# Kernel tuning notes

Measured on AMD Instinct MI355X. Metric: run time of the kernel, lower is better.

## Reference

```python
import jax, jax.numpy as jnp
import numpy as np

N_NODES = 100000
N_EDGES = 1600000
F_IN = 65
HIDDEN = 128
N_CLASSES = 32
NEG_SLOPE = 0.2


def _gat_conv(x0, src, dst, W, a_src, a_dst, b):
    """Single-head GAT-style conv: gather over edges, segment softmax, scatter-add."""
    h = x0 @ W                                  # [N, C]
    s = h @ a_src                                # [N]
    d = h @ a_dst                                # [N]
    e = jax.nn.leaky_relu(s[src] + d[dst], NEG_SLOPE)   # [E]
    m = jax.ops.segment_max(e, dst, num_segments=N_NODES)
    m = jnp.where(jnp.isfinite(m), m, 0.0)
    ex = jnp.exp(e - m[dst])                     # [E]
    denom = jax.ops.segment_sum(ex, dst, num_segments=N_NODES)
    alpha = ex / (denom[dst] + 1e-16)            # [E]
    out = jax.ops.segment_sum(h[src] * alpha[:, None], dst, num_segments=N_NODES)
    return out + b                               # [N, C]


def setup_inputs() -> dict:
    key = jax.random.key(0)
    ks = jax.random.split(key, 12)
    sc_in = 1.0 / np.sqrt(F_IN)
    sc_h = 1.0 / np.sqrt(HIDDEN)
    return {
        "x": jax.random.normal(ks[0], (N_NODES, F_IN), dtype=jnp.float32),
        "edge_index": jax.random.randint(ks[1], (2, N_EDGES), 0, N_NODES, dtype=jnp.int64),
        "W_mlp": jax.random.normal(ks[2], (F_IN, HIDDEN), dtype=jnp.float32) * sc_in,
        "b_mlp": jnp.zeros((HIDDEN,), dtype=jnp.float32),
        "W1": jax.random.normal(ks[3], (HIDDEN, N_CLASSES), dtype=jnp.float32) * sc_h,
        "a1_src": jax.random.normal(ks[4], (N_CLASSES,), dtype=jnp.float32) * 0.1,
        "a1_dst": jax.random.normal(ks[5], (N_CLASSES,), dtype=jnp.float32) * 0.1,
        "b1": jnp.zeros((N_CLASSES,), dtype=jnp.float32),
        "W2": jax.random.normal(ks[6], (HIDDEN, N_CLASSES), dtype=jnp.float32) * sc_h,
        "a2_src": jax.random.normal(ks[7], (N_CLASSES,), dtype=jnp.float32) * 0.1,
        "a2_dst": jax.random.normal(ks[8], (N_CLASSES,), dtype=jnp.float32) * 0.1,
        "b2": jnp.zeros((N_CLASSES,), dtype=jnp.float32),
    }


def reference(x, edge_index, W_mlp, b_mlp, W1, a1_src, a1_dst, b1, W2, a2_src, a2_dst, b2):
    src, dst = edge_index[0], edge_index[1]
    x0 = jax.nn.relu(x @ W_mlp + b_mlp)                      # [N, H]
    x1 = jax.nn.relu(_gat_conv(x0, src, dst, W1, a1_src, a1_dst, b1))  # [N, C]
    # dropout is identity in eval mode
    x2 = _gat_conv(x0, src, dst, W2, a2_src, a2_dst, b2)     # [N, C]
    x3 = jnp.max(x0, axis=-1, keepdims=True)                 # [N, 1]
    lngal_out = jnp.concatenate((x1, x2, x3), axis=-1) + x   # [N, 2C+1] == [N, F]
    return jax.nn.log_softmax(lngal_out, axis=1)
```

## Files before the change

### kernel.cpp

```cpp
#include <hip/hip_runtime.h>
#include <hip/hip_bf16.h>

#define NN 100000
#define NE 1600000
#define FIN 65
#define HID 128
#define NC 32
#define OUTC 65
#define NBUCK 391
#define CHUNKS 400
#define CH 4000
#define ESTRIDE 5120
#define NODE_BLOCKS 1563

typedef __attribute__((ext_vector_type(8))) short s8v;
typedef __attribute__((ext_vector_type(4))) float f4v;
#define MFMA16(a, b, c) __builtin_amdgcn_mfma_f32_16x16x32_bf16(a, b, c, 0, 0, 0)

__device__ __forceinline__ float lrelu(float v){ return v > 0.f ? v : 0.2f * v; }
__device__ __forceinline__ short f2bs(float f){
  unsigned u = __float_as_uint(f);
  u += 0x7fffu + ((u >> 16) & 1u);
  return (short)(u >> 16);
}
__device__ __forceinline__ float bfu_lo(unsigned u){ return __uint_as_float(u << 16); }
__device__ __forceinline__ float bfu_hi(unsigned u){ return __uint_as_float(u & 0xffff0000u); }

__global__ __launch_bounds__(256) void k_prep(
    const float* __restrict__ Wmlp, const float* __restrict__ W1,
    const float* __restrict__ W2, short* __restrict__ wbg,
    int* __restrict__ bcursor)
{
  const int i = blockIdx.x * 256 + threadIdx.x;
  if (blockIdx.x == 0)
    for (int t = threadIdx.x; t < NBUCK; t += 256) bcursor[t] = 0;
  {
    const int j = i & 7, l = (i >> 3) & 63, nt = (i >> 9) & 7, t = i >> 12;
    const int k = t * 32 + ((l >> 4) << 3) + j;
    const int col = (nt << 4) + (l & 15);
    wbg[i] = f2bs(Wmlp[k * HID + col]);
  }
  {
    const int j = i & 7, l = (i >> 3) & 63, nt = (i >> 9) & 3, t = i >> 11;
    const int k = t * 32 + ((l >> 4) << 3) + j;
    const int col = (nt << 4) + (l & 15);
    wbg[8192 + i] = f2bs(col < NC ? W1[k * NC + col] : W2[k * NC + col - NC]);
  }
}

__global__ __launch_bounds__(256) void k_main(
    const float* __restrict__ x, const short* __restrict__ wbg,
    const float* __restrict__ Wmlp, const float* __restrict__ bmlp,
    const float* __restrict__ a1s, const float* __restrict__ a1d,
    const float* __restrict__ a2s, const float* __restrict__ a2d,
    const int* __restrict__ ei,
    unsigned short* __restrict__ hb16,
    float* __restrict__ sd2, float* __restrict__ dd2,
    float* __restrict__ out,
    int* __restrict__ bcursor, int* __restrict__ ebuf)
{
  __shared__ alignas(16) char smem[28416];
  const int tid = threadIdx.x;

  if (blockIdx.x >= NODE_BLOCKS) {
    const int cb = blockIdx.x - NODE_BLOCKS;
    int* lh = (int*)smem;
    int* lbase = lh + NBUCK;
    for (int i = tid; i < NBUCK; i += 256) lh[i] = 0;
    __syncthreads();
    const int4* s4 = (const int4*)ei + cb * (CH / 4);
    const int4* d4 = (const int4*)(ei + NE) + cb * (CH / 4);
    for (int i = tid; i < CH / 4; i += 256) {
      int4 v = d4[i];
      atomicAdd(&lh[v.x >> 8], 1);
      atomicAdd(&lh[v.y >> 8], 1);
      atomicAdd(&lh[v.z >> 8], 1);
      atomicAdd(&lh[v.w >> 8], 1);
    }
    __syncthreads();
    for (int i = tid; i < NBUCK; i += 256) {
      int c = lh[i];
      lbase[i] = c ? (i * ESTRIDE + atomicAdd(&bcursor[i], c)) : 0;
      lh[i] = 0;
    }
    __syncthreads();
    for (int i = tid; i < CH / 4; i += 256) {
      int4 sv = s4[i];
      int4 dv = d4[i];
      int b, r;
      b = dv.x >> 8; r = atomicAdd(&lh[b], 1); ebuf[lbase[b] + r] = (sv.x << 8) | (dv.x & 255);
      b = dv.y >> 8; r = atomicAdd(&lh[b], 1); ebuf[lbase[b] + r] = (sv.y << 8) | (dv.y & 255);
      b = dv.z >> 8; r = atomicAdd(&lh[b], 1); ebuf[lbase[b] + r] = (sv.z << 8) | (dv.z & 255);
      b = dv.w >> 8; r = atomicAdd(&lh[b], 1); ebuf[lbase[b] + r] = (sv.w << 8) | (dv.w & 255);
    }
    return;
  }

  short* xbf = (short*)smem;
  short* x0b = (short*)(smem + 9216);
  float* xc64 = (float*)(smem + 26624);
  float* w64 = (float*)(smem + 26880);
  float* bmv = (float*)(smem + 27392);
  float* avv = (float*)(smem + 27904);

  const int base = blockIdx.x * 64;

  if (tid < 128) { w64[tid] = Wmlp[64 * HID + tid]; bmv[tid] = bmlp[tid]; }
  else if (tid < 160) {
    const int q = tid - 128;
    avv[q] = a1s[q]; avv[32 + q] = a1d[q]; avv[64 + q] = a2s[q]; avv[96 + q] = a2d[q];
  }
  for (int i = tid; i < 64 * 65; i += 256) {
    const int r = i / 65, c = i - r * 65;
    const int node = base + r;
    const float v = (node < NN) ? x[(size_t)node * FIN + c] : 0.f;
    if (c == 64) xc64[r] = v; else xbf[r * 72 + c] = f2bs(v);
  }
  __syncthreads();

  const int w = tid >> 6, lane = tid & 63;
  const int g = lane >> 4, q = lane & 15;
  const int rowA = w * 16 + q;
  const int rowD0 = w * 16 + g * 4;
  const s8v* wv8 = (const s8v*)wbg;

  const s8v a0 = *(const s8v*)&xbf[rowA * 72 + g * 8];
  const s8v a1 = *(const s8v*)&xbf[rowA * 72 + 32 + g * 8];

  f4v acc[8];
  #pragma unroll
  for (int nt = 0; nt < 8; ++nt) acc[nt] = (f4v){0.f, 0.f, 0.f, 0.f};
  #pragma unroll
  for (int nt = 0; nt < 8; ++nt) {
    const s8v b0 = wv8[nt * 64 + lane];
    const s8v b1 = wv8[(8 + nt) * 64 + lane];
    acc[nt] = MFMA16(a0, b0, acc[nt]);
    acc[nt] = MFMA16(a1, b1, acc[nt]);
  }

  float xc[4];
  #pragma unroll
  for (int r = 0; r < 4; ++r) xc[r] = xc64[rowD0 + r];
  float rmax[4] = {0.f, 0.f, 0.f, 0.f};
  #pragma unroll
  for (int nt = 0; nt < 8; ++nt) {
    const int col = nt * 16 + q;
    const float wvv = w64[col], bv = bmv[col];
    #pragma unroll
    for (int r = 0; r < 4; ++r) {
      const float v = fmaxf(fmaf(xc[r], wvv, acc[nt][r]) + bv, 0.f);
      rmax[r] = fmaxf(rmax[r], v);
      x0b[(rowD0 + r) * 136 + col] = f2bs(v);
    }
  }
  #pragma unroll
  for (int off = 1; off < 16; off <<= 1)
    #pragma unroll
    for (int r = 0; r < 4; ++r) rmax[r] = fmaxf(rmax[r], __shfl_xor(rmax[r], off));
  if (q == 0) {
    #pragma unroll
    for (int r = 0; r < 4; ++r) {
      const int node = base + rowD0 + r;
      if (node < NN) out[(size_t)node * OUTC + 64] = rmax[r];
    }
  }

  s8v af[4];
  #pragma unroll
  for (int t = 0; t < 4; ++t)
    af[t] = *(const s8v*)&x0b[rowA * 136 + t * 32 + g * 8];
  f4v hacc[4];
  #pragma unroll
  for (int nt = 0; nt < 4; ++nt) hacc[nt] = (f4v){0.f, 0.f, 0.f, 0.f};
  #pragma unroll
  for (int nt = 0; nt < 4; ++nt)
    #pragma unroll
    for (int t = 0; t < 4; ++t)
      hacc[nt] = MFMA16(af[t], wv8[1024 + (t * 4 + nt) * 64 + lane], hacc[nt]);

  float s1p[4], d1p[4], s2p[4], d2p[4];
  #pragma unroll
  for (int r = 0; r < 4; ++r) {
    s1p[r] = hacc[0][r] * avv[q]        + hacc[1][r] * avv[16 + q];
    d1p[r] = hacc[0][r] * avv[32 + q]   + hacc[1][r] * avv[48 + q];
    s2p[r] = hacc[2][r] * avv[64 + q]   + hacc[3][r] * avv[80 + q];
    d2p[r] = hacc[2][r] * avv[96 + q]   + hacc[3][r] * avv[112 + q];
  }
  #pragma unroll
  for (int off = 1; off < 16; off <<= 1) {
    #pragma unroll
    for (int r = 0; r < 4; ++r) {
      s1p[r] += __shfl_xor(s1p[r], off);
      d1p[r] += __shfl_xor(d1p[r], off);
      s2p[r] += __shfl_xor(s2p[r], off);
      d2p[r] += __shfl_xor(d2p[r], off);
    }
  }
  #pragma unroll
  for (int r = 0; r < 4; ++r) {
    const int node = base + rowD0 + r;
    if (node < NN) {
      #pragma unroll
      for (int nt = 0; nt < 4; ++nt)
        hb16[(size_t)node * 64 + nt * 16 + q] = (unsigned short)f2bs(hacc[nt][r]);
      if (q == 0) {
        *(float2*)&sd2[(size_t)node * 2] = make_float2(s1p[r], s2p[r]);
        *(float2*)&dd2[(size_t)node * 2] = make_float2(d1p[r], d2p[r]);
      }
    }
  }
}

__global__ __launch_bounds__(256) void k_csr(const int* __restrict__ bcursor,
                                             const int* __restrict__ ebuf,
                                             int* __restrict__ rpp,
                                             int* __restrict__ csrc)
{
  __shared__ int lh[256];
  __shared__ int wsum[4];
  const int b = blockIdx.x;
  const int e0 = b * ESTRIDE;
  const int cntb = bcursor[b];
  const int t = threadIdx.x;

  lh[t] = 0;
  __syncthreads();
  for (int i = t; i < cntb; i += 256)
    atomicAdd(&lh[ebuf[e0 + i] & 255], 1);
  __syncthreads();

  const int lane = t & 63;
  const int wid = t >> 6;
  int v = lh[t];
  const int orig = v;
  for (int off = 1; off < 64; off <<= 1) {
    int tm = __shfl_up(v, off);
    if (lane >= off) v += tm;
  }
  if (lane == 63) wsum[wid] = v;
  __syncthreads();
  int add = 0;
  for (int ww = 0; ww < wid; ++ww) add += wsum[ww];
  const int ex = v + add - orig;

  const int nb0 = b << 8;
  if (nb0 + t < NN) rpp[nb0 + t] = ((e0 + ex) << 8) | orig;
  __syncthreads();
  lh[t] = ex;
  __syncthreads();
  for (int i = t; i < cntb; i += 256) {
    int p = ebuf[e0 + i];
    int r = atomicAdd(&lh[p & 255], 1);
    csrc[e0 + r] = ((unsigned)p) >> 8;
  }
}

__global__ __launch_bounds__(256) void k_conv(
    const int* __restrict__ rpp, const int* __restrict__ csrc,
    const unsigned short* __restrict__ hb16,
    const float* __restrict__ sd2, const float* __restrict__ dd2,
    const float* __restrict__ x,
    const float* __restrict__ b1, const float* __restrict__ b2,
    float* __restrict__ out)
{
  const int wid = threadIdx.x >> 6;
  const int lane = threadIdx.x & 63;
  const int half = lane >> 5;
  const int hl = lane & 31;
  const int sub = hl >> 3;
  const int cg8 = hl & 7;
  const int conv = cg8 >> 2;

  const int node = blockIdx.x * 8 + wid * 2 + half;

  const int rv = rpp[node];
  const int base = ((unsigned)rv) >> 8;
  const int cnt = rv & 255;
  const float2 dnv = *(const float2*)&dd2[(size_t)node * 2];

  const char* hbp = (const char*)hb16;
  float a[8] = {0.f, 0.f, 0.f, 0.f, 0.f, 0.f, 0.f, 0.f};
  float den = 0.f;

  for (int chunk = 0; chunk < cnt; chunk += 32) {
    const int rem = min(cnt - chunk, 32);

    int sE = 0;
    float w1v = 0.f, w2v = 0.f;
    if (hl < rem) {
      sE = csrc[base + chunk + hl];
      const float2 sv = *(const float2*)&sd2[(size_t)sE * 2];
      w1v = __expf(lrelu(sv.x + dnv.x));
      w2v = __expf(lrelu(sv.y + dnv.y));
    }
    float d1 = w1v, d2 = w2v;
    #pragma unroll
    for (int off = 1; off < 32; off <<= 1) {
      d1 += __shfl_xor(d1, off);
      d2 += __shfl_xor(d2, off);
    }
    den += conv ? d2 : d1;

    for (int i0 = 0; i0 < rem; i0 += 4) {
      const int src = half * 32 + i0 + sub;
      const int s = __shfl(sE, src);
      const float wa = __shfl(w1v, src);
      const float wb = __shfl(w2v, src);
      const float w = conv ? wb : wa;
      const uint4 pv = *(const uint4*)(hbp + ((size_t)s << 7) + cg8 * 16);
      a[0] = fmaf(w, bfu_lo(pv.x), a[0]);
      a[1] = fmaf(w, bfu_hi(pv.x), a[1]);
      a[2] = fmaf(w, bfu_lo(pv.y), a[2]);
      a[3] = fmaf(w, bfu_hi(pv.y), a[3]);
      a[4] = fmaf(w, bfu_lo(pv.z), a[4]);
      a[5] = fmaf(w, bfu_hi(pv.z), a[5]);
      a[6] = fmaf(w, bfu_lo(pv.w), a[6]);
      a[7] = fmaf(w, bfu_hi(pv.w), a[7]);
    }
  }

  #pragma unroll
  for (int j = 0; j < 8; ++j) {
    a[j] += __shfl_xor(a[j], 8);
    a[j] += __shfl_xor(a[j], 16);
  }

  const int ch = cg8 * 8;
  const float rden = 1.f / (den + 1e-16f);
  const float* bp = conv ? (b2 + ch - 32) : (b1 + ch);
  const float4 bva = *(const float4*)bp;
  const float4 bvb = *(const float4*)(bp + 4);
  float v[8];
  v[0] = a[0] * rden + bva.x; v[1] = a[1] * rden + bva.y;
  v[2] = a[2] * rden + bva.z; v[3] = a[3] * rden + bva.w;
  v[4] = a[4] * rden + bvb.x; v[5] = a[5] * rden + bvb.y;
  v[6] = a[6] * rden + bvb.z; v[7] = a[7] * rden + bvb.w;
  if (conv == 0) {
    #pragma unroll
    for (int j = 0; j < 8; ++j) v[j] = fmaxf(v[j], 0.f);
  }
  const float* xr = x + (size_t)node * OUTC;
  float* row = out + (size_t)node * OUTC;
  const float4 xa = *(const float4*)&xr[ch];
  const float4 xb = *(const float4*)&xr[ch + 4];
  v[0] += xa.x; v[1] += xa.y; v[2] += xa.z; v[3] += xa.w;
  v[4] += xb.x; v[5] += xb.y; v[6] += xb.z; v[7] += xb.w;
  const float v64 = row[64] + xr[64];

  float mx = v[0];
  #pragma unroll
  for (int j = 1; j < 8; ++j) mx = fmaxf(mx, v[j]);
  #pragma unroll
  for (int off = 1; off < 8; off <<= 1) mx = fmaxf(mx, __shfl_xor(mx, off));
  mx = fmaxf(mx, v64);
  float sm = 0.f;
  #pragma unroll
  for (int j = 0; j < 8; ++j) sm += __expf(v[j] - mx);
  #pragma unroll
  for (int off = 1; off < 8; off <<= 1) sm += __shfl_xor(sm, off);
  sm += __expf(v64 - mx);
  const float ls = __logf(sm) + mx;

  if (sub == 0) {
    *(float4*)&row[ch]     = make_float4(v[0] - ls, v[1] - ls, v[2] - ls, v[3] - ls);
    *(float4*)&row[ch + 4] = make_float4(v[4] - ls, v[5] - ls, v[6] - ls, v[7] - ls);
    if (hl == 0) row[64] = v64 - ls;
  }
}

extern "C" void kernel_launch(void* const* d_in, const int* in_sizes, int n_in,
                              void* d_out, int out_size, void* d_ws, size_t ws_size,
                              hipStream_t stream)
{
  const float* x    = (const float*)d_in[0];
  const int*   ei   = (const int*)d_in[1];
  const float* Wmlp = (const float*)d_in[2];
  const float* bmlp = (const float*)d_in[3];
  const float* W1   = (const float*)d_in[4];
  const float* a1s  = (const float*)d_in[5];
  const float* a1d  = (const float*)d_in[6];
  const float* b1   = (const float*)d_in[7];
  const float* W2   = (const float*)d_in[8];
  const float* a2s  = (const float*)d_in[9];
  const float* a2d  = (const float*)d_in[10];
  const float* b2   = (const float*)d_in[11];
  float* out = (float*)d_out;

  unsigned short* hb16 = (unsigned short*)d_ws;
  float* sd2 = (float*)(hb16 + (size_t)NN * 64);
  float* dd2 = sd2 + (size_t)2 * NN;
  int* ebuf   = (int*)(dd2 + (size_t)2 * NN);
  int* csrc   = ebuf + (size_t)NBUCK * ESTRIDE;
  int* rpp    = csrc + (size_t)NBUCK * ESTRIDE;
  int* bcursor= rpp + NBUCK * 256;
  short* wbg  = (short*)(bcursor + NBUCK);

  k_prep<<<32, 256, 0, stream>>>(Wmlp, W1, W2, wbg, bcursor);

  k_main<<<NODE_BLOCKS + CHUNKS, 256, 0, stream>>>(
      x, wbg, Wmlp, bmlp, a1s, a1d, a2s, a2d, ei,
      hb16, sd2, dd2, out, bcursor, ebuf);

  k_csr<<<NBUCK, 256, 0, stream>>>(bcursor, ebuf, rpp, csrc);

  k_conv<<<NN / 8, 256, 0, stream>>>(rpp, csrc, hb16, sd2, dd2, x, b1, b2, out);
}
```

Measured before the change: 107.5 us.

## Retune edge chunking, vectorize x loads, and remap conv lanes to 8-byte gathers

Halves the edge bucket chunk size (more, smaller chunks) and vectorizes the x tile load with float4 reads plus a multiply-shift divide-by-65 on full blocks. The aggregation kernel now gives each lane 4 channels with 8-byte gathers, 2 edges per step across 16 lanes instead of 4 edges across 8 lanes. It packs both attention weights into one bf16 pair so each edge needs one shuffle instead of two. This cuts the accumulator registers and cross-lane reductions, but rounding the weights to bf16 loses precision and the loads are narrower.

```diff
diff --git a/kernel.cpp b/kernel.cpp
--- a/kernel.cpp
+++ b/kernel.cpp
@@ -8,8 +8,8 @@
 #define NC 32
 #define OUTC 65
 #define NBUCK 391
-#define CHUNKS 400
-#define CH 4000
+#define CHUNKS 800
+#define CH 2000
 #define ESTRIDE 5120
 #define NODE_BLOCKS 1563
 
@@ -110,11 +110,27 @@
     const int q = tid - 128;
     avv[q] = a1s[q]; avv[32 + q] = a1d[q]; avv[64 + q] = a2s[q]; avv[96 + q] = a2d[q];
   }
-  for (int i = tid; i < 64 * 65; i += 256) {
-    const int r = i / 65, c = i - r * 65;
-    const int node = base + r;
-    const float v = (node < NN) ? x[(size_t)node * FIN + c] : 0.f;
-    if (c == 64) xc64[r] = v; else xbf[r * 72 + c] = f2bs(v);
+  if (base + 64 <= NN) {
+    const float4* xsrc = (const float4*)(x + (size_t)base * FIN);
+    for (int i = tid; i < 1040; i += 256) {
+      const float4 v = xsrc[i];
+      const float vv[4] = {v.x, v.y, v.z, v.w};
+      const int f0 = i * 4;
+      #pragma unroll
+      for (int u = 0; u < 4; ++u) {
+        const int ff = f0 + u;
+        const int r = (int)(((unsigned)ff * 64528u) >> 22);
+        const int c = ff - r * 65;
+        if (c == 64) xc64[r] = vv[u]; else xbf[r * 72 + c] = f2bs(vv[u]);
+      }
+    }
+  } else {
+    for (int i = tid; i < 64 * 65; i += 256) {
+      const int r = i / 65, c = i - r * 65;
+      const int node = base + r;
+      const float v = (node < NN) ? x[(size_t)node * FIN + c] : 0.f;
+      if (c == 64) xc64[r] = v; else xbf[r * 72 + c] = f2bs(v);
+    }
   }
   __syncthreads();
 
@@ -167,16 +183,16 @@
 
   s8v af[4];
   #pragma unroll
-  for (int t = 0; t < 4; ++t)
-    af[t] = *(const s8v*)&x0b[rowA * 136 + t * 32 + g * 8];
+  for (int t2 = 0; t2 < 4; ++t2)
+    af[t2] = *(const s8v*)&x0b[rowA * 136 + t2 * 32 + g * 8];
   f4v hacc[4];
   #pragma unroll
   for (int nt = 0; nt < 4; ++nt) hacc[nt] = (f4v){0.f, 0.f, 0.f, 0.f};
   #pragma unroll
   for (int nt = 0; nt < 4; ++nt)
     #pragma unroll
-    for (int t = 0; t < 4; ++t)
-      hacc[nt] = MFMA16(af[t], wv8[1024 + (t * 4 + nt) * 64 + lane], hacc[nt]);
+    for (int t2 = 0; t2 < 4; ++t2)
+      hacc[nt] = MFMA16(af[t2], wv8[1024 + (t2 * 4 + nt) * 64 + lane], hacc[nt]);
 
   float s1p[4], d1p[4], s2p[4], d2p[4];
   #pragma unroll
@@ -267,9 +283,9 @@
   const int lane = threadIdx.x & 63;
   const int half = lane >> 5;
   const int hl = lane & 31;
-  const int sub = hl >> 3;
-  const int cg8 = hl & 7;
-  const int conv = cg8 >> 2;
+  const int eg = hl >> 4;
+  const int cg = hl & 15;
+  const int conv = cg >> 3;
 
   const int node = blockIdx.x * 8 + wid * 2 + half;
 
@@ -279,7 +295,7 @@
   const float2 dnv = *(const float2*)&dd2[(size_t)node * 2];
 
   const char* hbp = (const char*)hb16;
-  float a[8] = {0.f, 0.f, 0.f, 0.f, 0.f, 0.f, 0.f, 0.f};
+  float a0 = 0.f, a1 = 0.f, a2 = 0.f, a3 = 0.f;
   float den = 0.f;
 
   for (int chunk = 0; chunk < cnt; chunk += 32) {
@@ -301,70 +317,63 @@
     }
     den += conv ? d2 : d1;
 
-    for (int i0 = 0; i0 < rem; i0 += 4) {
-      const int src = half * 32 + i0 + sub;
-      const int s = __shfl(sE, src);
-      const float wa = __shfl(w1v, src);
-      const float wb = __shfl(w2v, src);
-      const float w = conv ? wb : wa;
-      const uint4 pv = *(const uint4*)(hbp + ((size_t)s << 7) + cg8 * 16);
-      a[0] = fmaf(w, bfu_lo(pv.x), a[0]);
-      a[1] = fmaf(w, bfu_hi(pv.x), a[1]);
-      a[2] = fmaf(w, bfu_lo(pv.y), a[2]);
-      a[3] = fmaf(w, bfu_hi(pv.y), a[3]);
-      a[4] = fmaf(w, bfu_lo(pv.z), a[4]);
-      a[5] = fmaf(w, bfu_hi(pv.z), a[5]);
-      a[6] = fmaf(w, bfu_lo(pv.w), a[6]);
-      a[7] = fmaf(w, bfu_hi(pv.w), a[7]);
-    }
-  }
-
-  #pragma unroll
-  for (int j = 0; j < 8; ++j) {
-    a[j] += __shfl_xor(a[j], 8);
-    a[j] += __shfl_xor(a[j], 16);
-  }
-
-  const int ch = cg8 * 8;
+    const int wpk = (int)((((unsigned)(unsigned short)f2bs(w2v)) << 16) |
+                           (unsigned)(unsigned short)f2bs(w1v));
+
+    for (int i0 = 0; i0 < rem; i0 += 8) {
+      #pragma unroll
+      for (int u = 0; u < 4; ++u) {
+        const int i = i0 + u * 2 + eg;
+        const int src = half * 32 + i;
+        const int s = __shfl(sE, src);
+        const unsigned wp = (unsigned)__shfl(wpk, src);
+        const float w = conv ? bfu_hi(wp) : bfu_lo(wp);
+        const uint2 pv = *(const uint2*)(hbp + ((size_t)s << 7) + cg * 8);
+        a0 = fmaf(w, bfu_lo(pv.x), a0);
+        a1 = fmaf(w, bfu_hi(pv.x), a1);
+        a2 = fmaf(w, bfu_lo(pv.y), a2);
+        a3 = fmaf(w, bfu_hi(pv.y), a3);
+      }
+    }
+  }
+
+  a0 += __shfl_xor(a0, 16);
+  a1 += __shfl_xor(a1, 16);
+  a2 += __shfl_xor(a2, 16);
+  a3 += __shfl_xor(a3, 16);
+
+  const int ch = cg * 4;
   const float rden = 1.f / (den + 1e-16f);
-  const float* bp = conv ? (b2 + ch - 32) : (b1 + ch);
-  const float4 bva = *(const float4*)bp;
-  const float4 bvb = *(const float4*)(bp + 4);
-  float v[8];
-  v[0] = a[0] * rden + bva.x; v[1] = a[1] * rden + bva.y;
-  v[2] = a[2] * rden + bva.z; v[3] = a[3] * rden + bva.w;
-  v[4] = a[4] * rden + bvb.x; v[5] = a[5] * rden + bvb.y;
-  v[6] = a[6] * rden + bvb.z; v[7] = a[7] * rden + bvb.w;
+  float v0 = a0 * rden, v1 = a1 * rden, v2 = a2 * rden, v3 = a3 * rden;
   if (conv == 0) {
-    #pragma unroll
-    for (int j = 0; j < 8; ++j) v[j] = fmaxf(v[j], 0.f);
+    const float4 bv = *(const float4*)&b1[ch];
+    v0 = fmaxf(v0 + bv.x, 0.f);
+    v1 = fmaxf(v1 + bv.y, 0.f);
+    v2 = fmaxf(v2 + bv.z, 0.f);
+    v3 = fmaxf(v3 + bv.w, 0.f);
+  } else {
+    const float4 bv = *(const float4*)&b2[ch - 32];
+    v0 += bv.x; v1 += bv.y; v2 += bv.z; v3 += bv.w;
   }
   const float* xr = x + (size_t)node * OUTC;
   float* row = out + (size_t)node * OUTC;
-  const float4 xa = *(const float4*)&xr[ch];
-  const float4 xb = *(const float4*)&xr[ch + 4];
-  v[0] += xa.x; v[1] += xa.y; v[2] += xa.z; v[3] += xa.w;
-  v[4] += xb.x; v[5] += xb.y; v[6] += xb.z; v[7] += xb.w;
+  const float4 xr4 = *(const float4*)&xr[ch];
+  v0 += xr4.x; v1 += xr4.y; v2 += xr4.z; v3 += xr4.w;
   const float v64 = row[64] + xr[64];
 
-  float mx = v[0];
-  #pragma unroll
-  for (int j = 1; j < 8; ++j) mx = fmaxf(mx, v[j]);
-  #pragma unroll
-  for (int off = 1; off < 8; off <<= 1) mx = fmaxf(mx, __shfl_xor(mx, off));
+  float mx = fmaxf(fmaxf(v0, v1), fmaxf(v2, v3));
+  #pragma unroll
+  for (int off = 1; off < 16; off <<= 1) mx = fmaxf(mx, __shfl_xor(mx, off));
   mx = fmaxf(mx, v64);
-  float sm = 0.f;
-  #pragma unroll
-  for (int j = 0; j < 8; ++j) sm += __expf(v[j] - mx);
-  #pragma unroll
-  for (int off = 1; off < 8; off <<= 1) sm += __shfl_xor(sm, off);
+  float sm = __expf(v0 - mx) + __expf(v1 - mx) + __expf(v2 - mx) + __expf(v3 - mx);
+  #pragma unroll
+  for (int off = 1; off < 16; off <<= 1) sm += __shfl_xor(sm, off);
   sm += __expf(v64 - mx);
-  const float ls = __logf(sm) + mx;
-
-  if (sub == 0) {
-    *(float4*)&row[ch]     = make_float4(v[0] - ls, v[1] - ls, v[2] - ls, v[3] - ls);
-    *(float4*)&row[ch + 4] = make_float4(v[4] - ls, v[5] - ls, v[6] - ls, v[7] - ls);
-    if (hl == 0) row[64] = v64 - ls;
+  const float ls = __logf(sm);
+
+  if (eg == 0) {
+    *(float4*)&row[ch] = make_float4(v0 - mx - ls, v1 - mx - ls, v2 - mx - ls, v3 - mx - ls);
+    if (hl == 0) row[64] = v64 - mx - ls;
   }
 }
 
```

Result: slower. 117.5 us (+9.3%).
